# Optimization experiments

Hardware: AMD Instinct MI355X
Metric: run time of the kernel (lower is better)

The kernel has to match this reference:

```python
import jax, jax.numpy as jnp
import numpy as np

B, V, D = 512, 50000, 512   # batch, vocab, embedding_dim
T, P, L, PL = 4, 16, 8, 32  # max_types, max_paths, max_pathlen, max_prop_len
OUT = 300


def masked_softmax(x):
    # zeros are treated as padding: add -9999 before softmax
    return jax.nn.softmax(x + jnp.where(x == 0, -9999.0, 0.0), axis=-1)


def cosine(a, b, eps=1e-8):
    na = jnp.maximum(jnp.linalg.norm(a, axis=1), eps)
    nb = jnp.maximum(jnp.linalg.norm(b, axis=1), eps)
    return jnp.sum(a * b, axis=1) / (na * nb)


def setup_inputs() -> dict:
    key = jax.random.key(0)
    ks = jax.random.split(key, 10)
    nodes = jax.random.randint(ks[0], (B, 2), 0, V)
    features = jax.random.randint(ks[1], (B, 2, T, P, L), 0, V)
    prop_nodes = jax.random.randint(ks[2], (B, 2), 0, V)
    prop_features = jax.random.randint(ks[3], (B, 2, 3, PL), 0, V)
    emb = jax.random.normal(ks[4], (V, D), dtype=jnp.float32)
    W_out = jax.random.normal(ks[5], (OUT, 2 * D), dtype=jnp.float32) * (1.0 / np.sqrt(2 * D))
    b_out = jnp.zeros((OUT,), dtype=jnp.float32)
    v = jnp.full((L,), 1.0 / L, dtype=jnp.float32)
    w_rootpath = jnp.array([0.25], dtype=jnp.float32)
    w_children = jnp.array([0.25], dtype=jnp.float32)
    w_obj_neighbours = jnp.array([0.25], dtype=jnp.float32)
    prop_weight = jnp.array([0.33], dtype=jnp.float32)
    domain_weight = jnp.array([0.33], dtype=jnp.float32)
    return dict(nodes=nodes, features=features, prop_nodes=prop_nodes,
                prop_features=prop_features, emb=emb, W_out=W_out, b_out=b_out,
                v=v, w_rootpath=w_rootpath, w_children=w_children,
                w_obj_neighbours=w_obj_neighbours, prop_weight=prop_weight,
                domain_weight=domain_weight)


def reference(nodes, features, prop_nodes, prop_features, emb, W_out, b_out,
              v, w_rootpath, w_children, w_obj_neighbours, prop_weight,
              domain_weight):
    results = []
    for i in range(2):  # the two siamese branches
        node_emb = emb[nodes[:, i]]                      # [B, D]
        feature_emb = emb[features[:, i]]                # [B, T, P, L, D]
        # score each path: dot every token with the node embedding, sum over pathlen
        path_weights = jnp.einsum('bd,btpld->btp', node_emb, feature_emb)  # [B,T,P]
        best = jnp.argmax(path_weights, axis=-1)         # [B, T]
        best_path = jnp.take_along_axis(
            feature_emb, best[:, :, None, None, None], axis=2).squeeze(2)  # [B,T,L,D]
        node_weights = masked_softmax(
            jnp.einsum('bd,btld->btl', node_emb, best_path))               # [B,T,L]
        attended = node_weights[..., None] * best_path                     # [B,T,L,D]
        dwp = jnp.einsum('l,btld->btd', v, attended)                       # [B,T,D]
        w_data = 1.0 - w_rootpath - w_children - w_obj_neighbours
        context = (w_rootpath * dwp[:, 0] + w_children * dwp[:, 1]
                   + w_obj_neighbours * dwp[:, 2] + w_data * dwp[:, 3])    # [B,D]
        contextual = jnp.concatenate([node_emb, context], axis=1)          # [B,2D]
        results.append(contextual @ W_out.T + b_out)                       # [B,300]
    sim_ent = cosine(results[0], results[1])                               # [B]
    # property branch (prop_nodes non-empty here)
    agg = emb[prop_features].sum(axis=-2)                                  # [B,2,3,D]
    sim_prop = (prop_weight * cosine(agg[:, 0, 0], agg[:, 1, 0])
                + domain_weight * cosine(agg[:, 0, 1], agg[:, 1, 1])
                + (1.0 - prop_weight - domain_weight) * cosine(agg[:, 0, 2], agg[:, 1, 2]))
    return jnp.concatenate([sim_ent, sim_prop])                            # [2B]
```

## Files before the change

### kernel.cpp

```cpp
#include <hip/hip_runtime.h>
#include <math.h>

#define B_ 512
#define V_ 50000
#define D_ 512
#define T_ 4
#define P_ 16
#define L_ 8
#define OUT_ 300
#define NBI 1024
#define NG  4096
#define NSLOT 524288
#define NPROPB 1536
#define CAP 40

typedef float f32x4 __attribute__((ext_vector_type(4)));

__global__ __launch_bounds__(256) void kprep(
    const int* __restrict__ features, int* __restrict__ counts,
    int* __restrict__ inv,
    const int* __restrict__ nodes, const float* __restrict__ emb,
    float* __restrict__ narr)
{
    const int blk = blockIdx.x;
    const int tid = threadIdx.x;
    if (blk < NSLOT / 256) {
        const int slot = blk * 256 + tid;
        const int row  = features[slot];
        const int pos  = atomicAdd(&counts[row], 1);
        if (pos < CAP) inv[row * CAP + pos] = slot;
    } else {
        const int bi = blk - NSLOT / 256;
        const float2 r = *(const float2*)(emb + (size_t)nodes[bi] * D_ + 2 * tid);
        *(float2*)(narr + (size_t)bi * D_ + 2 * tid) = r;
    }
}

__global__ __launch_bounds__(256) void kdh_dots_prop(
    const float* __restrict__ emb, const float* __restrict__ narr,
    const int* __restrict__ counts, const int* __restrict__ inv,
    float* __restrict__ sarr,
    const int* __restrict__ pf, float* __restrict__ pprt)
{
    const int blk = blockIdx.x;
    const int tid = threadIdx.x;

    __shared__ float4 lA[128], lB[128];
    __shared__ float  redp[2][3];

    if (blk < NPROPB) {
        const int bj  = blk;
        const int b   = bj / 3, j = bj % 3;
        const int d4   = tid & 127;
        const int half = tid >> 7;

        const int base0 = ((b * 2 + 0) * 3 + j) * 32;
        const int base1 = ((b * 2 + 1) * 3 + j) * 32;

        float4 accA = {0,0,0,0}, accB = {0,0,0,0};
        #pragma unroll 4
        for (int k = half; k < 32; k += 2) {
            const int ia = pf[base0 + k];
            const int ib = pf[base1 + k];
            const float4 ra = *(const float4*)(emb + (size_t)ia * D_ + 4 * d4);
            const float4 rb = *(const float4*)(emb + (size_t)ib * D_ + 4 * d4);
            accA.x += ra.x; accA.y += ra.y; accA.z += ra.z; accA.w += ra.w;
            accB.x += rb.x; accB.y += rb.y; accB.z += rb.z; accB.w += rb.w;
        }
        if (half == 1) { lA[d4] = accA; lB[d4] = accB; }
        __syncthreads();

        float pab = 0.f, paa = 0.f, pbb = 0.f;
        if (half == 0) {
            const float4 oA = lA[d4], oB = lB[d4];
            const float ax = accA.x + oA.x, ay = accA.y + oA.y;
            const float az = accA.z + oA.z, aw = accA.w + oA.w;
            const float bx = accB.x + oB.x, by = accB.y + oB.y;
            const float bz = accB.z + oB.z, bw = accB.w + oB.w;
            pab = ax*bx + ay*by + az*bz + aw*bw;
            paa = ax*ax + ay*ay + az*az + aw*aw;
            pbb = bx*bx + by*by + bz*bz + bw*bw;
        }
        #pragma unroll
        for (int off = 32; off; off >>= 1) {
            pab += __shfl_down(pab, off);
            paa += __shfl_down(paa, off);
            pbb += __shfl_down(pbb, off);
        }
        if ((tid & 63) == 0 && tid < 128) {
            redp[tid >> 6][0] = pab; redp[tid >> 6][1] = paa; redp[tid >> 6][2] = pbb;
        }
        __syncthreads();
        if (tid == 0) {
            pprt[bj * 3 + 0] = redp[0][0] + redp[1][0];
            pprt[bj * 3 + 1] = redp[0][1] + redp[1][1];
            pprt[bj * 3 + 2] = redp[0][2] + redp[1][2];
        }
        return;
    }

    const int wid = tid >> 6, lane = tid & 63;
    const int row = (blk - NPROPB) * 4 + wid;
    const int en  = min(counts[row], CAP);
    if (en == 0) return;
    const int base = row * CAP;

    const f32x4* rp4 = (const f32x4*)(emb + (size_t)row * D_ + lane * 8);
    const f32x4 r0 = __builtin_nontemporal_load(rp4);
    const f32x4 r1 = __builtin_nontemporal_load(rp4 + 1);

    const int grp = lane >> 4;
    const int sub = lane & 15;
    const int eperm = (grp == 1) ? 2 : (grp == 2) ? 1 : grp;

    for (int e = 0; e < en; e += 8) {
        const bool half2 = (e + 4) < en;
        int  s0[4], s1[4]; bool v0[4], v1[4];
        #pragma unroll
        for (int k = 0; k < 4; ++k) {
            v0[k] = (e + k) < en;
            s0[k] = inv[base + (v0[k] ? (e + k) : (en - 1))];
        }
        #pragma unroll
        for (int k = 0; k < 4; ++k) {
            v1[k] = (e + 4 + k) < en;
            s1[k] = inv[base + (v1[k] ? (e + 4 + k) : (en - 1))];
        }

        f32x4 A0[4], A1[4], B0[4], B1[4];
        #pragma unroll
        for (int k = 0; k < 4; ++k) {
            const f32x4* q = (const f32x4*)(narr + (size_t)(s0[k] >> 9) * D_ + lane * 8);
            A0[k] = q[0]; A1[k] = q[1];
        }
        if (half2) {
            #pragma unroll
            for (int k = 0; k < 4; ++k) {
                const f32x4* q = (const f32x4*)(narr + (size_t)(s1[k] >> 9) * D_ + lane * 8);
                B0[k] = q[0]; B1[k] = q[1];
            }
        }

        float d[4];
        #pragma unroll
        for (int k = 0; k < 4; ++k)
            d[k] = r0.x*A0[k].x + r0.y*A0[k].y + r0.z*A0[k].z + r0.w*A0[k].w
                 + r1.x*A1[k].x + r1.y*A1[k].y + r1.z*A1[k].z + r1.w*A1[k].w;
        {
            const bool b32 = (lane & 32) != 0;
            float c01 = (b32 ? d[1] : d[0]) + __shfl_xor(b32 ? d[0] : d[1], 32);
            float c23 = (b32 ? d[3] : d[2]) + __shfl_xor(b32 ? d[2] : d[3], 32);
            const bool b16 = (lane & 16) != 0;
            float c = (b16 ? c23 : c01) + __shfl_xor(b16 ? c01 : c23, 16);
            c += __shfl_xor(c, 8);
            c += __shfl_xor(c, 4);
            c += __shfl_xor(c, 2);
            c += __shfl_xor(c, 1);
            if (sub == 0 && v0[eperm]) sarr[s0[eperm]] = c;
        }
        if (half2) {
            float g[4];
            #pragma unroll
            for (int k = 0; k < 4; ++k)
                g[k] = r0.x*B0[k].x + r0.y*B0[k].y + r0.z*B0[k].z + r0.w*B0[k].w
                     + r1.x*B1[k].x + r1.y*B1[k].y + r1.z*B1[k].z + r1.w*B1[k].w;
            const bool b32 = (lane & 32) != 0;
            float c01 = (b32 ? g[1] : g[0]) + __shfl_xor(b32 ? g[0] : g[1], 32);
            float c23 = (b32 ? g[3] : g[2]) + __shfl_xor(b32 ? g[2] : g[3], 32);
            const bool b16 = (lane & 16) != 0;
            float c = (b16 ? c23 : c01) + __shfl_xor(b16 ? c01 : c23, 16);
            c += __shfl_xor(c, 8);
            c += __shfl_xor(c, 4);
            c += __shfl_xor(c, 2);
            c += __shfl_xor(c, 1);
            if (sub == 0 && v1[eperm]) sarr[s1[eperm]] = c;
        }
    }
}

__global__ __launch_bounds__(256) void kef_sel_ctx(
    const float* __restrict__ sarr, const int* __restrict__ features,
    const int* __restrict__ nodes, const float* __restrict__ emb,
    const float* __restrict__ v, const float* __restrict__ w_rp,
    const float* __restrict__ w_ch, const float* __restrict__ w_on,
    float* __restrict__ cont,
    const float* __restrict__ W, float4* __restrict__ Wtv)
{
    const int tid = threadIdx.x;
    if (blockIdx.x >= NBI) {
        const int o = blockIdx.x - NBI;
        const float4 w = *(const float4*)(W + (size_t)o * 1024 + 4 * tid);
        Wtv[(size_t)tid * OUT_ + o] = w;
        return;
    }

    const int bi  = blockIdx.x;
    const int wid = tid >> 6, lane = tid & 63;
    const int g = bi * 4 + wid;
    const int t = wid;

    __shared__ int   s_idx[32];
    __shared__ float s_coef[32];

    float bv = -1e30f; int bix = 0x7fffffff;
    if (lane < P_) {
        const float* sp = sarr + (size_t)g * 128 + lane * 8;
        const float4 x0 = ((const float4*)sp)[0];
        const float4 x1 = ((const float4*)sp)[1];
        bv = x0.x + x0.y + x0.z + x0.w + x1.x + x1.y + x1.z + x1.w;
        bix = lane;
    }
    #pragma unroll
    for (int off = 8; off; off >>= 1) {
        const float ov = __shfl_down(bv, off);
        const int   oi = __shfl_down(bix, off);
        if (ov > bv || (ov == bv && oi < bix)) { bv = ov; bix = oi; }
    }
    const int bp = __shfl(bix, 0);

    float sv = 0.f;
    if (lane < L_) sv = sarr[(size_t)g * 128 + bp * 8 + lane];
    float x = sv + (sv == 0.0f ? -9999.0f : 0.0f);
    float m = x;
    #pragma unroll
    for (int off = 4; off; off >>= 1) m = fmaxf(m, __shfl_xor(m, off));
    const float e = expf(x - m);
    float sum = e;
    #pragma unroll
    for (int off = 4; off; off >>= 1) sum += __shfl_xor(sum, off);

    if (lane < L_) {
        const float wr = w_rp[0], wc = w_ch[0], wo = w_on[0];
        const float tw = (t == 0) ? wr : (t == 1) ? wc : (t == 2) ? wo
                                       : (1.0f - wr - wc - wo);
        s_coef[wid * 8 + lane] = tw * v[lane] * (e / sum);
        s_idx [wid * 8 + lane] = features[(size_t)g * 128 + bp * 8 + lane];
    }
    __syncthreads();

    float2 c = {0.f, 0.f};
    #pragma unroll 8
    for (int r = 0; r < 32; ++r) {
        const int   idx = s_idx[r];
        const float cf  = s_coef[r];
        const float2 rr = *(const float2*)(emb + (size_t)idx * D_ + 2 * tid);
        c.x += cf * rr.x;
        c.y += cf * rr.y;
    }
    const float2 nn = *(const float2*)(emb + (size_t)nodes[bi] * D_ + 2 * tid);
    float* cp = cont + (size_t)bi * 1024;
    *(float2*)(cp + 2 * tid)       = nn;
    *(float2*)(cp + 512 + 2 * tid) = c;
}

__global__ __launch_bounds__(256) void kg_gemm_cos(
    const float* __restrict__ cont, const float4* __restrict__ Wtv,
    const float* __restrict__ bias, const float* __restrict__ pprt,
    const float* __restrict__ pw_, const float* __restrict__ dw_,
    float* __restrict__ out)
{
    const int bb  = blockIdx.x;
    const int tid = threadIdx.x;

    if (bb >= B_ / 2) {
        const int b = (bb - B_ / 2) * 256 + tid;
        if (b < B_) {
            float cosv[3];
            #pragma unroll
            for (int j = 0; j < 3; ++j) {
                const float ab = pprt[(b * 3 + j) * 3 + 0];
                const float aa = pprt[(b * 3 + j) * 3 + 1];
                const float bv = pprt[(b * 3 + j) * 3 + 2];
                const float na = fmaxf(sqrtf(aa), 1e-8f);
                const float nb = fmaxf(sqrtf(bv), 1e-8f);
                cosv[j] = ab / (na * nb);
            }
            const float pw = pw_[0], dw = dw_[0];
            out[B_ + b] = pw * cosv[0] + dw * cosv[1] + (1.0f - pw - dw) * cosv[2];
        }
        return;
    }

    const int wid = tid >> 6, lane = tid & 63;

    __shared__ float4 cs[1024];
    __shared__ float  red[4][6];

    const float* cb = cont + (size_t)bb * 4 * 1024;
    for (int idx = tid; idx < 4096; idx += 256) {
        const int vv = idx & 3, k = idx >> 2;
        ((float*)&cs[k])[vv] = cb[vv * 1024 + k];
    }
    __syncthreads();

    float p[6] = {0,0,0,0,0,0};
    #pragma unroll
    for (int pass = 0; pass < 2; ++pass) {
        const int o = tid + pass * 256;
        if (o < OUT_) {
            float4 acc = {0,0,0,0};
            const float4* wp = Wtv + o;
            #pragma unroll 4
            for (int k4 = 0; k4 < 256; ++k4) {
                const float4 wv = wp[(size_t)k4 * OUT_];
                const float4 c0 = cs[4*k4+0];
                const float4 c1 = cs[4*k4+1];
                const float4 c2 = cs[4*k4+2];
                const float4 c3 = cs[4*k4+3];
                acc.x += c0.x*wv.x + c1.x*wv.y + c2.x*wv.z + c3.x*wv.w;
                acc.y += c0.y*wv.x + c1.y*wv.y + c2.y*wv.z + c3.y*wv.w;
                acc.z += c0.z*wv.x + c1.z*wv.y + c2.z*wv.z + c3.z*wv.w;
                acc.w += c0.w*wv.x + c1.w*wv.y + c2.w*wv.z + c3.w*wv.w;
            }
            const float bo = bias[o];
            const float r0 = acc.x + bo, r1 = acc.y + bo;
            const float r2 = acc.z + bo, r3 = acc.w + bo;
            p[0] += r0 * r1; p[1] += r0 * r0; p[2] += r1 * r1;
            p[3] += r2 * r3; p[4] += r2 * r2; p[5] += r3 * r3;
        }
    }
    #pragma unroll
    for (int q = 0; q < 6; ++q) {
        #pragma unroll
        for (int off = 32; off; off >>= 1) p[q] += __shfl_down(p[q], off);
    }
    if (lane == 0) {
        #pragma unroll
        for (int q = 0; q < 6; ++q) red[wid][q] = p[q];
    }
    __syncthreads();
    if (tid < 2) {
        const int j = tid;
        float ab = 0.f, aa = 0.f, bbv = 0.f;
        #pragma unroll
        for (int w2 = 0; w2 < 4; ++w2) {
            ab  += red[w2][j*3+0];
            aa  += red[w2][j*3+1];
            bbv += red[w2][j*3+2];
        }
        const float na = fmaxf(sqrtf(aa),  1e-8f);
        const float nb = fmaxf(sqrtf(bbv), 1e-8f);
        out[bb * 2 + j] = ab / (na * nb);
    }
}

extern "C" void kernel_launch(void* const* d_in, const int* in_sizes, int n_in,
                              void* d_out, int out_size, void* d_ws, size_t ws_size,
                              hipStream_t stream) {
    const int*   nodes   = (const int*)  d_in[0];
    const int*   features= (const int*)  d_in[1];
    const int*   propf   = (const int*)  d_in[3];
    const float* emb     = (const float*)d_in[4];
    const float* W_out   = (const float*)d_in[5];
    const float* b_out   = (const float*)d_in[6];
    const float* v       = (const float*)d_in[7];
    const float* w_rp    = (const float*)d_in[8];
    const float* w_ch    = (const float*)d_in[9];
    const float* w_on    = (const float*)d_in[10];
    const float* pw      = (const float*)d_in[11];
    const float* dw      = (const float*)d_in[12];
    float* out = (float*)d_out;

    char* ws = (char*)d_ws;
    size_t o = 0;
    auto alloc = [&](size_t bytes) { char* p = ws + o; o += (bytes + 1023) & ~(size_t)1023; return p; };
    int*   counts = (int*)  alloc(V_ * 4);
    float* sarr   = (float*)alloc((size_t)NSLOT * 4);
    float* pprt   = (float*)alloc(B_ * 3 * 3 * 4);
    char*  nw     = alloc((size_t)NBI * D_ * 4);
    char*  ic     = alloc((size_t)V_ * CAP * 4);
    float*  narr = (float*)nw;
    float4* Wtv  = (float4*)nw;
    int*    inv  = (int*)ic;
    float*  cont = (float*)ic;

    hipMemsetAsync(counts, 0, V_ * 4, stream);
    kprep       <<<NSLOT/256 + NBI,  256, 0, stream>>>(
                   features, counts, inv, nodes, emb, narr);
    kdh_dots_prop<<<NPROPB + V_/4,   256, 0, stream>>>(emb, narr, counts, inv,
                                                       sarr, propf, pprt);
    kef_sel_ctx <<<NBI + OUT_,       256, 0, stream>>>(sarr, features, nodes, emb,
                                                       v, w_rp, w_ch, w_on, cont,
                                                       W_out, Wtv);
    kg_gemm_cos <<<B_/2 + 2,         256, 0, stream>>>(cont, Wtv, b_out, pprt,
                                                       pw, dw, out);
}
```

Before: 210.3 us.

## Split fused prop/dots kernel and simplify dot loop to two entries per step

Splits the combined property-aggregation and inverse-index dot kernel into two separate launches. It also replaces the 8-wide batched gather with its permuted shuffle reduction by a simpler loop that handles two slots per iteration, using plain loads and a standard shuffle-down reduction. This cuts register pressure and code complexity. In exchange it adds a kernel launch, loses overlap between the two workloads, and exposes less memory-level parallelism per wave.

```diff
diff --git a/kernel.cpp b/kernel.cpp
--- a/kernel.cpp
+++ b/kernel.cpp
@@ -14,8 +14,6 @@
 #define NPROPB 1536
 #define CAP 40
 
-typedef float f32x4 __attribute__((ext_vector_type(4)));
-
 __global__ __launch_bounds__(256) void kprep(
     const int* __restrict__ features, int* __restrict__ counts,
     int* __restrict__ inv,
@@ -36,144 +34,103 @@
     }
 }
 
-__global__ __launch_bounds__(256) void kdh_dots_prop(
+__global__ __launch_bounds__(256) void kh1_prop(
+    const int* __restrict__ pf, const float* __restrict__ emb,
+    float* __restrict__ pprt)
+{
+    const int bj  = blockIdx.x;
+    const int b   = bj / 3, j = bj % 3;
+    const int tid = threadIdx.x;
+    const int d4   = tid & 127;
+    const int half = tid >> 7;
+
+    const int base0 = ((b * 2 + 0) * 3 + j) * 32;
+    const int base1 = ((b * 2 + 1) * 3 + j) * 32;
+
+    float4 accA = {0,0,0,0}, accB = {0,0,0,0};
+    #pragma unroll 4
+    for (int k = half; k < 32; k += 2) {
+        const int ia = pf[base0 + k];
+        const int ib = pf[base1 + k];
+        const float4 ra = *(const float4*)(emb + (size_t)ia * D_ + 4 * d4);
+        const float4 rb = *(const float4*)(emb + (size_t)ib * D_ + 4 * d4);
+        accA.x += ra.x; accA.y += ra.y; accA.z += ra.z; accA.w += ra.w;
+        accB.x += rb.x; accB.y += rb.y; accB.z += rb.z; accB.w += rb.w;
+    }
+
+    __shared__ float4 lA[128], lB[128];
+    __shared__ float  red[2][3];
+    if (half == 1) { lA[d4] = accA; lB[d4] = accB; }
+    __syncthreads();
+
+    float pab = 0.f, paa = 0.f, pbb = 0.f;
+    if (half == 0) {
+        const float4 oA = lA[d4], oB = lB[d4];
+        const float ax = accA.x + oA.x, ay = accA.y + oA.y;
+        const float az = accA.z + oA.z, aw = accA.w + oA.w;
+        const float bx = accB.x + oB.x, by = accB.y + oB.y;
+        const float bz = accB.z + oB.z, bw = accB.w + oB.w;
+        pab = ax*bx + ay*by + az*bz + aw*bw;
+        paa = ax*ax + ay*ay + az*az + aw*aw;
+        pbb = bx*bx + by*by + bz*bz + bw*bw;
+    }
+    #pragma unroll
+    for (int off = 32; off; off >>= 1) {
+        pab += __shfl_down(pab, off);
+        paa += __shfl_down(paa, off);
+        pbb += __shfl_down(pbb, off);
+    }
+    if ((tid & 63) == 0 && tid < 128) {
+        red[tid >> 6][0] = pab; red[tid >> 6][1] = paa; red[tid >> 6][2] = pbb;
+    }
+    __syncthreads();
+    if (tid == 0) {
+        pprt[bj * 3 + 0] = red[0][0] + red[1][0];
+        pprt[bj * 3 + 1] = red[0][1] + red[1][1];
+        pprt[bj * 3 + 2] = red[0][2] + red[1][2];
+    }
+}
+
+__global__ __launch_bounds__(256) void kd_dots(
     const float* __restrict__ emb, const float* __restrict__ narr,
     const int* __restrict__ counts, const int* __restrict__ inv,
-    float* __restrict__ sarr,
-    const int* __restrict__ pf, float* __restrict__ pprt)
-{
-    const int blk = blockIdx.x;
-    const int tid = threadIdx.x;
-
-    __shared__ float4 lA[128], lB[128];
-    __shared__ float  redp[2][3];
-
-    if (blk < NPROPB) {
-        const int bj  = blk;
-        const int b   = bj / 3, j = bj % 3;
-        const int d4   = tid & 127;
-        const int half = tid >> 7;
-
-        const int base0 = ((b * 2 + 0) * 3 + j) * 32;
-        const int base1 = ((b * 2 + 1) * 3 + j) * 32;
-
-        float4 accA = {0,0,0,0}, accB = {0,0,0,0};
-        #pragma unroll 4
-        for (int k = half; k < 32; k += 2) {
-            const int ia = pf[base0 + k];
-            const int ib = pf[base1 + k];
-            const float4 ra = *(const float4*)(emb + (size_t)ia * D_ + 4 * d4);
-            const float4 rb = *(const float4*)(emb + (size_t)ib * D_ + 4 * d4);
-            accA.x += ra.x; accA.y += ra.y; accA.z += ra.z; accA.w += ra.w;
-            accB.x += rb.x; accB.y += rb.y; accB.z += rb.z; accB.w += rb.w;
-        }
-        if (half == 1) { lA[d4] = accA; lB[d4] = accB; }
-        __syncthreads();
-
-        float pab = 0.f, paa = 0.f, pbb = 0.f;
-        if (half == 0) {
-            const float4 oA = lA[d4], oB = lB[d4];
-            const float ax = accA.x + oA.x, ay = accA.y + oA.y;
-            const float az = accA.z + oA.z, aw = accA.w + oA.w;
-            const float bx = accB.x + oB.x, by = accB.y + oB.y;
-            const float bz = accB.z + oB.z, bw = accB.w + oB.w;
-            pab = ax*bx + ay*by + az*bz + aw*bw;
-            paa = ax*ax + ay*ay + az*az + aw*aw;
-            pbb = bx*bx + by*by + bz*bz + bw*bw;
-        }
-        #pragma unroll
-        for (int off = 32; off; off >>= 1) {
-            pab += __shfl_down(pab, off);
-            paa += __shfl_down(paa, off);
-            pbb += __shfl_down(pbb, off);
-        }
-        if ((tid & 63) == 0 && tid < 128) {
-            redp[tid >> 6][0] = pab; redp[tid >> 6][1] = paa; redp[tid >> 6][2] = pbb;
-        }
-        __syncthreads();
-        if (tid == 0) {
-            pprt[bj * 3 + 0] = redp[0][0] + redp[1][0];
-            pprt[bj * 3 + 1] = redp[0][1] + redp[1][1];
-            pprt[bj * 3 + 2] = redp[0][2] + redp[1][2];
-        }
-        return;
-    }
-
+    float* __restrict__ sarr)
+{
+    const int tid = threadIdx.x;
     const int wid = tid >> 6, lane = tid & 63;
-    const int row = (blk - NPROPB) * 4 + wid;
+    const int row = blockIdx.x * 4 + wid;
     const int en  = min(counts[row], CAP);
     if (en == 0) return;
     const int base = row * CAP;
 
-    const f32x4* rp4 = (const f32x4*)(emb + (size_t)row * D_ + lane * 8);
-    const f32x4 r0 = __builtin_nontemporal_load(rp4);
-    const f32x4 r1 = __builtin_nontemporal_load(rp4 + 1);
-
-    const int grp = lane >> 4;
-    const int sub = lane & 15;
-    const int eperm = (grp == 1) ? 2 : (grp == 2) ? 1 : grp;
-
-    for (int e = 0; e < en; e += 8) {
-        const bool half2 = (e + 4) < en;
-        int  s0[4], s1[4]; bool v0[4], v1[4];
+    const float* rp = emb + (size_t)row * D_ + lane * 8;
+    const float4 r0 = ((const float4*)rp)[0];
+    const float4 r1 = ((const float4*)rp)[1];
+
+    for (int e = 0; e < en; e += 2) {
+        const int s0 = inv[base + e];
+        const int s1 = (e + 1 < en) ? inv[base + e + 1] : -1;
+        const float* q0 = narr + (size_t)(s0 >> 9) * D_ + lane * 8;
+        const float4 a0 = ((const float4*)q0)[0];
+        const float4 a1 = ((const float4*)q0)[1];
+        float d0 = r0.x*a0.x + r0.y*a0.y + r0.z*a0.z + r0.w*a0.w
+                 + r1.x*a1.x + r1.y*a1.y + r1.z*a1.z + r1.w*a1.w;
+        float d1 = 0.f;
+        if (s1 >= 0) {
+            const float* q1 = narr + (size_t)(s1 >> 9) * D_ + lane * 8;
+            const float4 b0 = ((const float4*)q1)[0];
+            const float4 b1 = ((const float4*)q1)[1];
+            d1 = r0.x*b0.x + r0.y*b0.y + r0.z*b0.z + r0.w*b0.w
+               + r1.x*b1.x + r1.y*b1.y + r1.z*b1.z + r1.w*b1.w;
+        }
         #pragma unroll
-        for (int k = 0; k < 4; ++k) {
-            v0[k] = (e + k) < en;
-            s0[k] = inv[base + (v0[k] ? (e + k) : (en - 1))];
-        }
-        #pragma unroll
-        for (int k = 0; k < 4; ++k) {
-            v1[k] = (e + 4 + k) < en;
-            s1[k] = inv[base + (v1[k] ? (e + 4 + k) : (en - 1))];
-        }
-
-        f32x4 A0[4], A1[4], B0[4], B1[4];
-        #pragma unroll
-        for (int k = 0; k < 4; ++k) {
-            const f32x4* q = (const f32x4*)(narr + (size_t)(s0[k] >> 9) * D_ + lane * 8);
-            A0[k] = q[0]; A1[k] = q[1];
-        }
-        if (half2) {
-            #pragma unroll
-            for (int k = 0; k < 4; ++k) {
-                const f32x4* q = (const f32x4*)(narr + (size_t)(s1[k] >> 9) * D_ + lane * 8);
-                B0[k] = q[0]; B1[k] = q[1];
-            }
-        }
-
-        float d[4];
-        #pragma unroll
-        for (int k = 0; k < 4; ++k)
-            d[k] = r0.x*A0[k].x + r0.y*A0[k].y + r0.z*A0[k].z + r0.w*A0[k].w
-                 + r1.x*A1[k].x + r1.y*A1[k].y + r1.z*A1[k].z + r1.w*A1[k].w;
-        {
-            const bool b32 = (lane & 32) != 0;
-            float c01 = (b32 ? d[1] : d[0]) + __shfl_xor(b32 ? d[0] : d[1], 32);
-            float c23 = (b32 ? d[3] : d[2]) + __shfl_xor(b32 ? d[2] : d[3], 32);
-            const bool b16 = (lane & 16) != 0;
-            float c = (b16 ? c23 : c01) + __shfl_xor(b16 ? c01 : c23, 16);
-            c += __shfl_xor(c, 8);
-            c += __shfl_xor(c, 4);
-            c += __shfl_xor(c, 2);
-            c += __shfl_xor(c, 1);
-            if (sub == 0 && v0[eperm]) sarr[s0[eperm]] = c;
-        }
-        if (half2) {
-            float g[4];
-            #pragma unroll
-            for (int k = 0; k < 4; ++k)
-                g[k] = r0.x*B0[k].x + r0.y*B0[k].y + r0.z*B0[k].z + r0.w*B0[k].w
-                     + r1.x*B1[k].x + r1.y*B1[k].y + r1.z*B1[k].z + r1.w*B1[k].w;
-            const bool b32 = (lane & 32) != 0;
-            float c01 = (b32 ? g[1] : g[0]) + __shfl_xor(b32 ? g[0] : g[1], 32);
-            float c23 = (b32 ? g[3] : g[2]) + __shfl_xor(b32 ? g[2] : g[3], 32);
-            const bool b16 = (lane & 16) != 0;
-            float c = (b16 ? c23 : c01) + __shfl_xor(b16 ? c01 : c23, 16);
-            c += __shfl_xor(c, 8);
-            c += __shfl_xor(c, 4);
-            c += __shfl_xor(c, 2);
-            c += __shfl_xor(c, 1);
-            if (sub == 0 && v1[eperm]) sarr[s1[eperm]] = c;
+        for (int off = 32; off; off >>= 1) {
+            d0 += __shfl_down(d0, off);
+            d1 += __shfl_down(d1, off);
+        }
+        if (lane == 0) {
+            sarr[s0] = d0;
+            if (s1 >= 0) sarr[s1] = d1;
         }
     }
 }
@@ -375,13 +332,13 @@
     float*  cont = (float*)ic;
 
     hipMemsetAsync(counts, 0, V_ * 4, stream);
-    kprep       <<<NSLOT/256 + NBI,  256, 0, stream>>>(
-                   features, counts, inv, nodes, emb, narr);
-    kdh_dots_prop<<<NPROPB + V_/4,   256, 0, stream>>>(emb, narr, counts, inv,
-                                                       sarr, propf, pprt);
-    kef_sel_ctx <<<NBI + OUT_,       256, 0, stream>>>(sarr, features, nodes, emb,
-                                                       v, w_rp, w_ch, w_on, cont,
-                                                       W_out, Wtv);
-    kg_gemm_cos <<<B_/2 + 2,         256, 0, stream>>>(cont, Wtv, b_out, pprt,
-                                                       pw, dw, out);
-}
+    kprep      <<<NSLOT/256 + NBI,  256, 0, stream>>>(
+                  features, counts, inv, nodes, emb, narr);
+    kh1_prop   <<<NPROPB,           256, 0, stream>>>(propf, emb, pprt);
+    kd_dots    <<<V_/4,             256, 0, stream>>>(emb, narr, counts, inv, sarr);
+    kef_sel_ctx<<<NBI + OUT_,       256, 0, stream>>>(sarr, features, nodes, emb,
+                                                      v, w_rp, w_ch, w_on, cont,
+                                                      W_out, Wtv);
+    kg_gemm_cos<<<B_/2 + 2,         256, 0, stream>>>(cont, Wtv, b_out, pprt,
+                                                      pw, dw, out);
+}
```

Result: faster. 203.0 us (-3.5%).
